# Performance work log

Hardware: AMD Instinct MI355X
Metric: run time of the kernel (lower is better)

The kernel has to match this reference:

```python
import jax, jax.numpy as jnp
import numpy as np

B, N, E, HID, ED, NH = 2, 10000, 160000, 128, 32, 8
HD = HID // NH  # head_dim = 16
EPS = 1e-5


def setup_inputs() -> dict:
    key = jax.random.key(0)
    ks = jax.random.split(key, 12)
    s = 0.05  # keep pre-tanh activations in a sane range
    return {
        "h": jax.random.normal(ks[0], (B, N, HID), jnp.float32),
        "edge_attr": jax.random.normal(ks[1], (B, E, ED), jnp.float32),
        "edge_index": jax.random.randint(ks[2], (E, 2), 0, N),
        "Wq": jax.random.normal(ks[3], (HID, HID), jnp.float32) * s,
        "bq": jnp.zeros((HID,), jnp.float32),
        "Wk": jax.random.normal(ks[4], (HID, HID), jnp.float32) * s,
        "bk": jnp.zeros((HID,), jnp.float32),
        "Wv": jax.random.normal(ks[5], (HID, HID), jnp.float32) * s,
        "bv": jnp.zeros((HID,), jnp.float32),
        "We": jax.random.normal(ks[6], (HID, ED), jnp.float32) * s,
        "be": jnp.zeros((HID,), jnp.float32),
        "attn_vec": jax.random.normal(ks[7], (NH, HD), jnp.float32) * 0.02,
        "Ws": jax.random.normal(ks[8], (HID, HID), jnp.float32) * s,
        "bs": jnp.zeros((HID,), jnp.float32),
        "Wa": jax.random.normal(ks[9], (HID, HID), jnp.float32) * s,
        "ba": jnp.zeros((HID,), jnp.float32),
        "ln_g": jnp.ones((HID,), jnp.float32),
        "ln_b": jnp.zeros((HID,), jnp.float32),
    }


def reference(h, edge_attr, edge_index, Wq, bq, Wk, bk, Wv, bv, We, be,
              attn_vec, Ws, bs, Wa, ba, ln_g, ln_b):
    src = edge_index[:, 0]
    dst = edge_index[:, 1]
    b, n, hid = h.shape
    e_cnt = src.shape[0]

    h_src = h[:, src, :]  # [B,E,HID]
    h_dst = h[:, dst, :]

    q = (h_dst @ Wq.T + bq).reshape(b, e_cnt, NH, HD)
    k = (h_src @ Wk.T + bk).reshape(b, e_cnt, NH, HD)
    v = (h_src @ Wv.T + bv).reshape(b, e_cnt, NH, HD)
    e = (edge_attr @ We.T + be).reshape(b, e_cnt, NH, HD)

    # GATv2-style scores: [B,E,NH]
    logits = jnp.einsum('behd,hd->beh', jnp.tanh(q + k + e), attn_vec)
    logits = logits / np.float32(np.sqrt(HD))

    # segment softmax over edges grouped by dst node (stable)
    lt = jnp.transpose(logits, (1, 0, 2))  # [E,B,NH]
    mx = jax.ops.segment_max(lt, dst, num_segments=n)  # [N,B,NH]
    ex = jnp.exp(lt - mx[dst])
    den = jax.ops.segment_sum(ex, dst, num_segments=n)
    alpha = jnp.transpose(ex / den[dst], (1, 0, 2))  # [B,E,NH]

    msg = (alpha[..., None] * (v + e)).reshape(b, e_cnt, hid)  # [B,E,HID]
    agg = jax.ops.segment_sum(jnp.transpose(msg, (1, 0, 2)), dst, num_segments=n)
    agg = jnp.transpose(agg, (1, 0, 2))  # [B,N,HID]

    update = (h @ Ws.T + bs) + (agg @ Wa.T + ba)
    x = h + jax.nn.gelu(update, approximate=False)  # dropout is identity in eval

    mu = jnp.mean(x, axis=-1, keepdims=True)
    var = jnp.var(x, axis=-1, keepdims=True)
    return (x - mu) / jnp.sqrt(var + EPS) * ln_g + ln_b
```

## Files before the change

kernel.cpp:

```cpp
#include <hip/hip_runtime.h>
#include <math.h>
#include <stdint.h>

#define B_   2
#define N_   10000
#define E_   160000
#define HID_ 128
#define ED_  32
#define NH_  8
#define HD_  16
#define ROWS_ (B_ * N_)

using half2_t = __attribute__((ext_vector_type(2))) _Float16;
using f16x8   = __attribute__((ext_vector_type(8))) _Float16;
using f32x4   = __attribute__((ext_vector_type(4))) float;

__device__ __forceinline__ half2_t f2h2(float a, float b) {
    return __builtin_bit_cast(half2_t, __builtin_amdgcn_cvt_pkrtz(a, b));
}
__device__ __forceinline__ uint32_t pkh2(float a, float b) {
    return __builtin_bit_cast(uint32_t, __builtin_amdgcn_cvt_pkrtz(a, b));
}


__global__ void zero_kernel(int* __restrict__ deg, int* __restrict__ cursor, int n) {
    int i = blockIdx.x * 256 + threadIdx.x;
    if (i < n) { deg[i] = 0; cursor[i] = 0; }
}

__global__ void hist_kernel(const int* __restrict__ ei, int* __restrict__ deg, int E) {
    int e = blockIdx.x * 256 + threadIdx.x;
    if (e < E) atomicAdd(&deg[ei[2 * e + 1]], 1);
}

__global__ __launch_bounds__(256) void scan_kernel(const int* __restrict__ deg,
                                                   int* __restrict__ off, int N) {
    __shared__ int sums[256];
    int t = threadIdx.x;
    int chunk = (N + 255) / 256;
    int s0 = t * chunk, s1 = min(N, s0 + chunk);
    int s = 0;
    for (int i = s0; i < s1; ++i) s += deg[i];
    sums[t] = s;
    __syncthreads();
    #pragma unroll
    for (int d = 1; d < 256; d <<= 1) {
        int v = (t >= d) ? sums[t - d] : 0;
        __syncthreads();
        sums[t] += v;
        __syncthreads();
    }
    if (t == 255) off[N] = sums[255];
    int run = sums[t] - s;
    for (int i = s0; i < s1; ++i) { off[i] = run; run += deg[i]; }
}

__global__ void fill_kernel(const int* __restrict__ ei, const int* __restrict__ off,
                            int* __restrict__ cursor, int* __restrict__ csr, int E) {
    int e = blockIdx.x * 256 + threadIdx.x;
    if (e < E) {
        int d = ei[2 * e + 1];
        int p = atomicAdd(&cursor[d], 1);
        csr[off[d] + p] = e;
    }
}


#define GM 64
#define LDA 68

__global__ __launch_bounds__(256) void qkvs_kernel(
    const float* __restrict__ h,
    const float* __restrict__ Wq, const float* __restrict__ bq,
    const float* __restrict__ Wk, const float* __restrict__ bk,
    const float* __restrict__ Wv, const float* __restrict__ bv,
    const float* __restrict__ Ws, const float* __restrict__ bs,
    const float* __restrict__ ba,
    float* __restrict__ Q, float* __restrict__ KV, float* __restrict__ S)
{
    __shared__ uint32_t As[GM * LDA];
    __shared__ uint32_t Bs[128 * LDA];
    __shared__ float bsm[128];

    int tid = threadIdx.x;
    int lane = tid & 63;
    int wave = tid >> 6;
    int row0 = blockIdx.x * GM;
    int J0 = blockIdx.y * 128;

    if (tid < 128) {
        int J = J0 + tid;
        float v;
        if (J < 128)      v = bq[J];
        else if (J < 256) v = bk[J - 128];
        else if (J < 384) v = bv[J - 256];
        else              v = bs[J - 384] + ba[J - 384];
        bsm[tid] = v;
    }

    for (int f = tid; f < GM * 32; f += 256) {
        int r = f >> 5, c4 = f & 31;
        long row = row0 + r;
        float4 hv = (row < ROWS_) ? *(const float4*)(h + row * HID_ + c4 * 4)
                                  : make_float4(0.f, 0.f, 0.f, 0.f);
        As[r * LDA + c4 * 2]     = pkh2(hv.x, hv.y);
        As[r * LDA + c4 * 2 + 1] = pkh2(hv.z, hv.w);
    }
    for (int f = tid; f < 128 * 32; f += 256) {
        int jr = f >> 5, c4 = f & 31;
        int J = J0 + jr;
        const float* Wp;
        if (J < 128)      Wp = Wq + (long)J * HID_;
        else if (J < 256) Wp = Wk + (long)(J - 128) * HID_;
        else if (J < 384) Wp = Wv + (long)(J - 256) * HID_;
        else              Wp = Ws + (long)(J - 384) * HID_;
        float4 wv = *(const float4*)(Wp + c4 * 4);
        Bs[jr * LDA + c4 * 2]     = pkh2(wv.x, wv.y);
        Bs[jr * LDA + c4 * 2 + 1] = pkh2(wv.z, wv.w);
    }
    __syncthreads();

    f32x4 acc[8];
    #pragma unroll
    for (int nt = 0; nt < 8; ++nt) {
        float c = bsm[nt * 16 + (lane & 15)];
        acc[nt] = (f32x4){ c, c, c, c };
    }

    int ar = wave * 16 + (lane & 15);
    #pragma unroll
    for (int ks = 0; ks < 4; ++ks) {
        f16x8 a = *(const f16x8*)(As + ar * LDA + ks * 16 + (lane >> 4) * 4);
        #pragma unroll
        for (int nt = 0; nt < 8; ++nt) {
            f16x8 b = *(const f16x8*)(Bs + (nt * 16 + (lane & 15)) * LDA + ks * 16 + (lane >> 4) * 4);
            acc[nt] = __builtin_amdgcn_mfma_f32_16x16x32_f16(a, b, acc[nt], 0, 0, 0);
        }
    }

    #pragma unroll
    for (int nt = 0; nt < 8; ++nt) {
        int J = J0 + nt * 16 + (lane & 15);
        long rbase = row0 + wave * 16 + (lane >> 4) * 4;
        #pragma unroll
        for (int r = 0; r < 4; ++r) {
            long row = rbase + r;
            if (row < ROWS_) {
                float v = acc[nt][r];
                if (J < 128)      Q[row * 128 + J] = v;
                else if (J < 256) KV[row * 256 + 2 * (J - 128)] = v;
                else if (J < 384) KV[row * 256 + 2 * (J - 256) + 1] = v;
                else              S[row * 128 + (J - 384)] = v;
            }
        }
    }
}

__global__ __launch_bounds__(256) void wa_kernel(
    const float* __restrict__ X, const float* __restrict__ Wa, float* __restrict__ A)
{
    __shared__ uint32_t As[GM * LDA];
    __shared__ uint32_t Bs[128 * LDA];

    int tid = threadIdx.x;
    int lane = tid & 63;
    int wave = tid >> 6;
    int row0 = blockIdx.x * GM;

    for (int f = tid; f < GM * 32; f += 256) {
        int r = f >> 5, c4 = f & 31;
        long row = row0 + r;
        float4 hv = (row < ROWS_) ? *(const float4*)(X + row * HID_ + c4 * 4)
                                  : make_float4(0.f, 0.f, 0.f, 0.f);
        As[r * LDA + c4 * 2]     = pkh2(hv.x, hv.y);
        As[r * LDA + c4 * 2 + 1] = pkh2(hv.z, hv.w);
    }
    for (int f = tid; f < 128 * 32; f += 256) {
        int jr = f >> 5, c4 = f & 31;
        float4 wv = *(const float4*)(Wa + (long)jr * HID_ + c4 * 4);
        Bs[jr * LDA + c4 * 2]     = pkh2(wv.x, wv.y);
        Bs[jr * LDA + c4 * 2 + 1] = pkh2(wv.z, wv.w);
    }
    __syncthreads();

    f32x4 acc[8];
    #pragma unroll
    for (int nt = 0; nt < 8; ++nt) acc[nt] = (f32x4){ 0.f, 0.f, 0.f, 0.f };

    int ar = wave * 16 + (lane & 15);
    #pragma unroll
    for (int ks = 0; ks < 4; ++ks) {
        f16x8 a = *(const f16x8*)(As + ar * LDA + ks * 16 + (lane >> 4) * 4);
        #pragma unroll
        for (int nt = 0; nt < 8; ++nt) {
            f16x8 b = *(const f16x8*)(Bs + (nt * 16 + (lane & 15)) * LDA + ks * 16 + (lane >> 4) * 4);
            acc[nt] = __builtin_amdgcn_mfma_f32_16x16x32_f16(a, b, acc[nt], 0, 0, 0);
        }
    }

    #pragma unroll
    for (int nt = 0; nt < 8; ++nt) {
        int J = nt * 16 + (lane & 15);
        long rbase = row0 + wave * 16 + (lane >> 4) * 4;
        #pragma unroll
        for (int r = 0; r < 4; ++r) {
            long row = rbase + r;
            if (row < ROWS_) A[row * 128 + J] = acc[nt][r];
        }
    }
}


template <int CTRL>
__device__ __forceinline__ float dpp_add(float x) {
    int y = __builtin_amdgcn_mov_dpp(__float_as_int(x), CTRL, 0xF, 0xF, true);
    return x + __int_as_float(y);
}
__device__ __forceinline__ float hsum16(float p) {
    p = dpp_add<0xB1>(p);
    p = dpp_add<0x4E>(p);
    p = dpp_add<0x141>(p);
    p = dpp_add<0x140>(p);
    return p;
}


#define NPB 2
#define CHUNK 64
#define EAS 20

__global__ __launch_bounds__(128) void node_kernel(
    const float* __restrict__ edge_attr, const int* __restrict__ ei,
    const float* __restrict__ Q, const float* __restrict__ KV,
    const float* __restrict__ We, const float* __restrict__ be,
    const float* __restrict__ attn_vec,
    const int* __restrict__ off, const int* __restrict__ csr,
    float* __restrict__ agg)
{
    int n0 = blockIdx.x * NPB;
    int b  = blockIdx.y;
    int j  = threadIdx.x;
    long bN = (long)b * N_;

    __shared__ int sL[CHUNK];
    __shared__ uint32_t eaL[CHUNK * EAS];

    half2_t we16[16];
    {
        const float4* We4 = (const float4*)(We + (long)j * ED_);
        #pragma unroll
        for (int c = 0; c < 8; ++c) {
            float4 w = We4[c];
            we16[2 * c]     = f2h2(w.x, w.y);
            we16[2 * c + 1] = f2h2(w.z, w.w);
        }
    }
    float bej = be[j];
    float avj = attn_vec[j] * 0.25f;

    float q0 = Q[(bN + n0 + 0) * 128 + j];
    float q1 = Q[(bN + n0 + 1) * 128 + j];

    int o0 = off[n0];
    int c1 = off[n0 + 1] - o0, c2 = off[n0 + 2] - o0;
    int total = c2;

    const float* eab = edge_attr + (long)b * E_ * ED_;
    const float* KVb = KV + bN * 256;

    float acc0 = 0.f, den0 = 0.f, acc1 = 0.f, den1 = 0.f;

    auto edge_body = [&](int i, float qg, float& accg, float& deng) {
        int s = sL[i];
        float2 kv = *(const float2*)(KVb + (long)s * 256 + 2 * j);
        const half2_t* ea = (const half2_t*)(eaL + i * EAS);
        float eja = bej, ejb = 0.f;
        #pragma unroll
        for (int c = 0; c < 8; ++c) {
            eja = __builtin_amdgcn_fdot2(we16[c], ea[c], eja, false);
            ejb = __builtin_amdgcn_fdot2(we16[c + 8], ea[c + 8], ejb, false);
        }
        float ej = eja + ejb;
        float y = qg + kv.x + ej;
        float t = 1.f - 2.f * __builtin_amdgcn_rcpf(__expf(2.f * y) + 1.f);
        float p = hsum16(t * avj);
        float ex = __expf(p);
        deng += ex;
        accg += ex * (kv.y + ej);
    };

    auto range_loop = [&](int lo, int hi, float qg, float& accg, float& deng) {
        int i = lo;
        for (; i + 3 < hi; i += 4) {
            edge_body(i, qg, accg, deng);
            edge_body(i + 1, qg, accg, deng);
            edge_body(i + 2, qg, accg, deng);
            edge_body(i + 3, qg, accg, deng);
        }
        for (; i < hi; ++i) edge_body(i, qg, accg, deng);
    };

    for (int tau = 0; tau < total; tau += CHUNK) {
        int rows = min(total - tau, CHUNK);
        __syncthreads();
        for (int t = j; t < rows; t += 128) {
            int e = csr[o0 + tau + t];
            sL[t] = ei[2 * e];
        }
        for (int idx = j; idx < rows * 8; idx += 128) {
            int r = idx >> 3, c = idx & 7;
            int e = csr[o0 + tau + r];
            float4 f = *(const float4*)(eab + (long)e * ED_ + c * 4);
            eaL[r * EAS + 2 * c]     = pkh2(f.x, f.y);
            eaL[r * EAS + 2 * c + 1] = pkh2(f.z, f.w);
        }
        __syncthreads();

        range_loop(max(0 - tau, 0),  min(c1 - tau, rows), q0, acc0, den0);
        range_loop(max(c1 - tau, 0), min(c2 - tau, rows), q1, acc1, den1);
    }

    agg[(bN + n0 + 0) * 128 + j] = (c1 > 0)  ? acc0 * __builtin_amdgcn_rcpf(den0) : 0.f;
    agg[(bN + n0 + 1) * 128 + j] = (c2 > c1) ? acc1 * __builtin_amdgcn_rcpf(den1) : 0.f;
}


__global__ __launch_bounds__(128) void final_kernel(
    const float* __restrict__ h, const float* __restrict__ S, const float* __restrict__ A,
    const float* __restrict__ ln_g, const float* __restrict__ ln_b,
    float* __restrict__ out)
{
    long row = blockIdx.x;
    int j = threadIdx.x;
    __shared__ float red[4];

    float upd = S[row * 128 + j] + A[row * 128 + j];
    float ge = 0.5f * upd * (1.f + erff(upd * 0.70710678118654752f));
    float x = h[row * 128 + j] + ge;

    float s = x, s2 = x * x;
    #pragma unroll
    for (int m = 1; m < 64; m <<= 1) { s += __shfl_xor(s, m); s2 += __shfl_xor(s2, m); }
    int wv = j >> 6;
    if ((j & 63) == 0) { red[wv] = s; red[2 + wv] = s2; }
    __syncthreads();
    float Sm = red[0] + red[1], S2m = red[2] + red[3];
    float mu = Sm * (1.f / 128.f);
    float var = S2m * (1.f / 128.f) - mu * mu;
    out[row * 128 + j] = (x - mu) * rsqrtf(var + 1e-5f) * ln_g[j] + ln_b[j];
}


extern "C" void kernel_launch(void* const* d_in, const int* in_sizes, int n_in,
                              void* d_out, int out_size, void* d_ws, size_t ws_size,
                              hipStream_t stream) {
    const float* h         = (const float*)d_in[0];
    const float* edge_attr = (const float*)d_in[1];
    const int*   ei        = (const int*)  d_in[2];
    const float* Wq = (const float*)d_in[3];
    const float* bq = (const float*)d_in[4];
    const float* Wk = (const float*)d_in[5];
    const float* bk = (const float*)d_in[6];
    const float* Wv = (const float*)d_in[7];
    const float* bv = (const float*)d_in[8];
    const float* We = (const float*)d_in[9];
    const float* be = (const float*)d_in[10];
    const float* attn_vec = (const float*)d_in[11];
    const float* Ws = (const float*)d_in[12];
    const float* bs = (const float*)d_in[13];
    const float* Wa = (const float*)d_in[14];
    const float* ba = (const float*)d_in[15];
    const float* ln_g = (const float*)d_in[16];
    const float* ln_b = (const float*)d_in[17];
    float* out = (float*)d_out;

    size_t p = 0;
    auto alloc = [&](size_t bytes) { size_t r = p; p += (bytes + 255) & ~(size_t)255; return r; };
    char* ws = (char*)d_ws;
    float* Q    = (float*)(ws + alloc((size_t)ROWS_ * 128 * 4));
    float* KV   = (float*)(ws + alloc((size_t)ROWS_ * 256 * 4));
    float* S    = (float*)(ws + alloc((size_t)ROWS_ * 128 * 4));
    float* agg  = (float*)(ws + alloc((size_t)ROWS_ * 128 * 4));
    int* deg    = (int*)(ws + alloc((size_t)N_ * 4));
    int* cursor = (int*)(ws + alloc((size_t)N_ * 4));
    int* off    = (int*)(ws + alloc((size_t)(N_ + 1) * 4));
    int* csr    = (int*)(ws + alloc((size_t)E_ * 4));
    float* A = Q;
    (void)ws_size;

    zero_kernel<<<(N_ + 255) / 256, 256, 0, stream>>>(deg, cursor, N_);
    hist_kernel<<<(E_ + 255) / 256, 256, 0, stream>>>(ei, deg, E_);
    scan_kernel<<<1, 256, 0, stream>>>(deg, off, N_);
    fill_kernel<<<(E_ + 255) / 256, 256, 0, stream>>>(ei, off, cursor, csr, E_);

    dim3 ggrid((ROWS_ + GM - 1) / GM, 4);
    qkvs_kernel<<<ggrid, 256, 0, stream>>>(h, Wq, bq, Wk, bk, Wv, bv, Ws, bs, ba,
                                           Q, KV, S);

    dim3 grid(N_ / NPB, B_);
    node_kernel<<<grid, 128, 0, stream>>>(edge_attr, ei, Q, KV, We, be, attn_vec,
                                          off, csr, agg);

    dim3 wgrid((ROWS_ + GM - 1) / GM, 1);
    wa_kernel<<<wgrid, 256, 0, stream>>>(agg, Wa, A);

    final_kernel<<<ROWS_, 128, 0, stream>>>(h, S, A, ln_g, ln_b, out);
}
```

Measured before the change: 177.5 us.

## Precompute edge projections with MFMA per batch and store K/V in fp16

Adds an MFMA-based eproj kernel that computes edge_attr @ We^T + be once per edge into an fp16 buffer, run per batch and followed by a per-batch node kernel. The node kernel no longer recomputes the 32-wide edge projection per edge per thread with fdot2. It reads a single fp16 value per edge instead. K/V are also stored as packed fp16, halving gather bandwidth, and the shared-memory chunk is enlarged. This trades per-edge ALU work for an extra 40MB-per-batch fp16 write and reread, extra launches, and reduced precision in the gathered values.

```diff
diff --git a/kernel.cpp b/kernel.cpp
--- a/kernel.cpp
+++ b/kernel.cpp
@@ -15,11 +15,11 @@
 using f16x8   = __attribute__((ext_vector_type(8))) _Float16;
 using f32x4   = __attribute__((ext_vector_type(4))) float;
 
-__device__ __forceinline__ half2_t f2h2(float a, float b) {
-    return __builtin_bit_cast(half2_t, __builtin_amdgcn_cvt_pkrtz(a, b));
-}
 __device__ __forceinline__ uint32_t pkh2(float a, float b) {
     return __builtin_bit_cast(uint32_t, __builtin_amdgcn_cvt_pkrtz(a, b));
+}
+__device__ __forceinline__ uint16_t f2h(float v) {
+    return __builtin_bit_cast(uint16_t, (_Float16)v);
 }
 
 
@@ -76,7 +76,7 @@
     const float* __restrict__ Wv, const float* __restrict__ bv,
     const float* __restrict__ Ws, const float* __restrict__ bs,
     const float* __restrict__ ba,
-    float* __restrict__ Q, float* __restrict__ KV, float* __restrict__ S)
+    float* __restrict__ Q, uint16_t* __restrict__ KVh, float* __restrict__ S)
 {
     __shared__ uint32_t As[GM * LDA];
     __shared__ uint32_t Bs[128 * LDA];
@@ -148,13 +148,150 @@
             if (row < ROWS_) {
                 float v = acc[nt][r];
                 if (J < 128)      Q[row * 128 + J] = v;
-                else if (J < 256) KV[row * 256 + 2 * (J - 128)] = v;
-                else if (J < 384) KV[row * 256 + 2 * (J - 256) + 1] = v;
+                else if (J < 256) KVh[row * 256 + 2 * (J - 128)] = f2h(v);
+                else if (J < 384) KVh[row * 256 + 2 * (J - 256) + 1] = f2h(v);
                 else              S[row * 128 + (J - 384)] = v;
             }
         }
     }
 }
+
+
+#define EM 64
+#define ELD 18
+
+__global__ __launch_bounds__(256) void eproj_kernel(
+    const float* __restrict__ ea,
+    const float* __restrict__ We, const float* __restrict__ be,
+    uint16_t* __restrict__ Ep)
+{
+    __shared__ uint32_t As[EM * ELD];
+    __shared__ uint32_t Bs[128 * ELD];
+    __shared__ float bsm[128];
+
+    int tid = threadIdx.x;
+    int lane = tid & 63;
+    int wave = tid >> 6;
+    long row0 = (long)blockIdx.x * EM;
+
+    if (tid < 128) bsm[tid] = be[tid];
+
+    for (int f = tid; f < EM * 8; f += 256) {
+        int r = f >> 3, c4 = f & 7;
+        float4 v = *(const float4*)(ea + (row0 + r) * ED_ + c4 * 4);
+        As[r * ELD + c4 * 2]     = pkh2(v.x, v.y);
+        As[r * ELD + c4 * 2 + 1] = pkh2(v.z, v.w);
+    }
+    for (int f = tid; f < 128 * 8; f += 256) {
+        int r = f >> 3, c4 = f & 7;
+        float4 v = *(const float4*)(We + (long)r * ED_ + c4 * 4);
+        Bs[r * ELD + c4 * 2]     = pkh2(v.x, v.y);
+        Bs[r * ELD + c4 * 2 + 1] = pkh2(v.z, v.w);
+    }
+    __syncthreads();
+
+    int ar = wave * 16 + (lane & 15);
+    f16x8 a = *(const f16x8*)(As + ar * ELD + (lane >> 4) * 4);
+    long rbase = row0 + wave * 16 + (lane >> 4) * 4;
+    #pragma unroll
+    for (int nt = 0; nt < 8; ++nt) {
+        float c = bsm[nt * 16 + (lane & 15)];
+        f32x4 acc = (f32x4){ c, c, c, c };
+        f16x8 b = *(const f16x8*)(Bs + (nt * 16 + (lane & 15)) * ELD + (lane >> 4) * 4);
+        acc = __builtin_amdgcn_mfma_f32_16x16x32_f16(a, b, acc, 0, 0, 0);
+        int pcol = nt * 16 + (lane & 15);
+        #pragma unroll
+        for (int r = 0; r < 4; ++r)
+            Ep[(rbase + r) * 128 + pcol] = f2h(acc[r]);
+    }
+}
+
+
+template <int CTRL>
+__device__ __forceinline__ float dpp_add(float x) {
+    int y = __builtin_amdgcn_mov_dpp(__float_as_int(x), CTRL, 0xF, 0xF, true);
+    return x + __int_as_float(y);
+}
+__device__ __forceinline__ float hsum16(float p) {
+    p = dpp_add<0xB1>(p);
+    p = dpp_add<0x4E>(p);
+    p = dpp_add<0x141>(p);
+    p = dpp_add<0x140>(p);
+    return p;
+}
+
+
+#define NPB 2
+#define CHUNK 128
+
+__global__ __launch_bounds__(128) void node_kernel(
+    const int* __restrict__ ei,
+    const float* __restrict__ Q, const uint32_t* __restrict__ KVp,
+    const uint16_t* __restrict__ Ep,
+    const float* __restrict__ attn_vec,
+    const int* __restrict__ off, const int* __restrict__ csr,
+    float* __restrict__ agg, int b)
+{
+    int n0 = blockIdx.x * NPB;
+    int j  = threadIdx.x;
+    long bN = (long)b * N_;
+
+    __shared__ int sL[CHUNK], eL[CHUNK];
+
+    float avj = attn_vec[j] * 0.25f;
+
+    float q0 = Q[(bN + n0 + 0) * 128 + j];
+    float q1 = Q[(bN + n0 + 1) * 128 + j];
+
+    int o0 = off[n0];
+    int c1 = off[n0 + 1] - o0, c2 = off[n0 + 2] - o0;
+    int total = c2;
+
+    const uint32_t* KVb = KVp + bN * 128;
+
+    float acc0 = 0.f, den0 = 0.f, acc1 = 0.f, den1 = 0.f;
+
+    auto edge_body = [&](int i, float qg, float& accg, float& deng) {
+        int s = sL[i], e = eL[i];
+        half2_t kv = __builtin_bit_cast(half2_t, KVb[(long)s * 128 + j]);
+        float ej = (float)__builtin_bit_cast(_Float16, Ep[(long)e * 128 + j]);
+        float y = qg + (float)kv.x + ej;
+        float t = 1.f - 2.f * __builtin_amdgcn_rcpf(__expf(2.f * y) + 1.f);
+        float p = hsum16(t * avj);
+        float ex = __expf(p);
+        deng += ex;
+        accg += ex * ((float)kv.y + ej);
+    };
+
+    auto range_loop = [&](int lo, int hi, float qg, float& accg, float& deng) {
+        int i = lo;
+        for (; i + 3 < hi; i += 4) {
+            edge_body(i, qg, accg, deng);
+            edge_body(i + 1, qg, accg, deng);
+            edge_body(i + 2, qg, accg, deng);
+            edge_body(i + 3, qg, accg, deng);
+        }
+        for (; i < hi; ++i) edge_body(i, qg, accg, deng);
+    };
+
+    for (int tau = 0; tau < total; tau += CHUNK) {
+        int rows = min(total - tau, CHUNK);
+        __syncthreads();
+        if (j < rows) {
+            int e = csr[o0 + tau + j];
+            eL[j] = e;
+            sL[j] = ei[2 * e];
+        }
+        __syncthreads();
+
+        range_loop(max(0 - tau, 0),  min(c1 - tau, rows), q0, acc0, den0);
+        range_loop(max(c1 - tau, 0), min(c2 - tau, rows), q1, acc1, den1);
+    }
+
+    agg[(bN + n0 + 0) * 128 + j] = (c1 > 0)  ? acc0 * __builtin_amdgcn_rcpf(den0) : 0.f;
+    agg[(bN + n0 + 1) * 128 + j] = (c2 > c1) ? acc1 * __builtin_amdgcn_rcpf(den1) : 0.f;
+}
+
 
 __global__ __launch_bounds__(256) void wa_kernel(
     const float* __restrict__ X, const float* __restrict__ Wa, float* __restrict__ A)
@@ -208,120 +345,6 @@
             if (row < ROWS_) A[row * 128 + J] = acc[nt][r];
         }
     }
-}
-
-
-template <int CTRL>
-__device__ __forceinline__ float dpp_add(float x) {
-    int y = __builtin_amdgcn_mov_dpp(__float_as_int(x), CTRL, 0xF, 0xF, true);
-    return x + __int_as_float(y);
-}
-__device__ __forceinline__ float hsum16(float p) {
-    p = dpp_add<0xB1>(p);
-    p = dpp_add<0x4E>(p);
-    p = dpp_add<0x141>(p);
-    p = dpp_add<0x140>(p);
-    return p;
-}
-
-
-#define NPB 2
-#define CHUNK 64
-#define EAS 20
-
-__global__ __launch_bounds__(128) void node_kernel(
-    const float* __restrict__ edge_attr, const int* __restrict__ ei,
-    const float* __restrict__ Q, const float* __restrict__ KV,
-    const float* __restrict__ We, const float* __restrict__ be,
-    const float* __restrict__ attn_vec,
-    const int* __restrict__ off, const int* __restrict__ csr,
-    float* __restrict__ agg)
-{
-    int n0 = blockIdx.x * NPB;
-    int b  = blockIdx.y;
-    int j  = threadIdx.x;
-    long bN = (long)b * N_;
-
-    __shared__ int sL[CHUNK];
-    __shared__ uint32_t eaL[CHUNK * EAS];
-
-    half2_t we16[16];
-    {
-        const float4* We4 = (const float4*)(We + (long)j * ED_);
-        #pragma unroll
-        for (int c = 0; c < 8; ++c) {
-            float4 w = We4[c];
-            we16[2 * c]     = f2h2(w.x, w.y);
-            we16[2 * c + 1] = f2h2(w.z, w.w);
-        }
-    }
-    float bej = be[j];
-    float avj = attn_vec[j] * 0.25f;
-
-    float q0 = Q[(bN + n0 + 0) * 128 + j];
-    float q1 = Q[(bN + n0 + 1) * 128 + j];
-
-    int o0 = off[n0];
-    int c1 = off[n0 + 1] - o0, c2 = off[n0 + 2] - o0;
-    int total = c2;
-
-    const float* eab = edge_attr + (long)b * E_ * ED_;
-    const float* KVb = KV + bN * 256;
-
-    float acc0 = 0.f, den0 = 0.f, acc1 = 0.f, den1 = 0.f;
-
-    auto edge_body = [&](int i, float qg, float& accg, float& deng) {
-        int s = sL[i];
-        float2 kv = *(const float2*)(KVb + (long)s * 256 + 2 * j);
-        const half2_t* ea = (const half2_t*)(eaL + i * EAS);
-        float eja = bej, ejb = 0.f;
-        #pragma unroll
-        for (int c = 0; c < 8; ++c) {
-            eja = __builtin_amdgcn_fdot2(we16[c], ea[c], eja, false);
-            ejb = __builtin_amdgcn_fdot2(we16[c + 8], ea[c + 8], ejb, false);
-        }
-        float ej = eja + ejb;
-        float y = qg + kv.x + ej;
-        float t = 1.f - 2.f * __builtin_amdgcn_rcpf(__expf(2.f * y) + 1.f);
-        float p = hsum16(t * avj);
-        float ex = __expf(p);
-        deng += ex;
-        accg += ex * (kv.y + ej);
-    };
-
-    auto range_loop = [&](int lo, int hi, float qg, float& accg, float& deng) {
-        int i = lo;
-        for (; i + 3 < hi; i += 4) {
-            edge_body(i, qg, accg, deng);
-            edge_body(i + 1, qg, accg, deng);
-            edge_body(i + 2, qg, accg, deng);
-            edge_body(i + 3, qg, accg, deng);
-        }
-        for (; i < hi; ++i) edge_body(i, qg, accg, deng);
-    };
-
-    for (int tau = 0; tau < total; tau += CHUNK) {
-        int rows = min(total - tau, CHUNK);
-        __syncthreads();
-        for (int t = j; t < rows; t += 128) {
-            int e = csr[o0 + tau + t];
-            sL[t] = ei[2 * e];
-        }
-        for (int idx = j; idx < rows * 8; idx += 128) {
-            int r = idx >> 3, c = idx & 7;
-            int e = csr[o0 + tau + r];
-            float4 f = *(const float4*)(eab + (long)e * ED_ + c * 4);
-            eaL[r * EAS + 2 * c]     = pkh2(f.x, f.y);
-            eaL[r * EAS + 2 * c + 1] = pkh2(f.z, f.w);
-        }
-        __syncthreads();
-
-        range_loop(max(0 - tau, 0),  min(c1 - tau, rows), q0, acc0, den0);
-        range_loop(max(c1 - tau, 0), min(c2 - tau, rows), q1, acc1, den1);
-    }
-
-    agg[(bN + n0 + 0) * 128 + j] = (c1 > 0)  ? acc0 * __builtin_amdgcn_rcpf(den0) : 0.f;
-    agg[(bN + n0 + 1) * 128 + j] = (c2 > c1) ? acc1 * __builtin_amdgcn_rcpf(den1) : 0.f;
 }
 
 
@@ -377,10 +400,11 @@
     size_t p = 0;
     auto alloc = [&](size_t bytes) { size_t r = p; p += (bytes + 255) & ~(size_t)255; return r; };
     char* ws = (char*)d_ws;
-    float* Q    = (float*)(ws + alloc((size_t)ROWS_ * 128 * 4));
-    float* KV   = (float*)(ws + alloc((size_t)ROWS_ * 256 * 4));
-    float* S    = (float*)(ws + alloc((size_t)ROWS_ * 128 * 4));
-    float* agg  = (float*)(ws + alloc((size_t)ROWS_ * 128 * 4));
+    float*    Q    = (float*)(ws + alloc((size_t)ROWS_ * 128 * 4));
+    uint16_t* KVh  = (uint16_t*)(ws + alloc((size_t)ROWS_ * 256 * 2));
+    float*    S    = (float*)(ws + alloc((size_t)ROWS_ * 128 * 4));
+    float*    agg  = (float*)(ws + alloc((size_t)ROWS_ * 128 * 4));
+    uint16_t* Ep   = (uint16_t*)(ws + alloc((size_t)E_ * 128 * 2));
     int* deg    = (int*)(ws + alloc((size_t)N_ * 4));
     int* cursor = (int*)(ws + alloc((size_t)N_ * 4));
     int* off    = (int*)(ws + alloc((size_t)(N_ + 1) * 4));
@@ -395,14 +419,16 @@
 
     dim3 ggrid((ROWS_ + GM - 1) / GM, 4);
     qkvs_kernel<<<ggrid, 256, 0, stream>>>(h, Wq, bq, Wk, bk, Wv, bv, Ws, bs, ba,
-                                           Q, KV, S);
-
-    dim3 grid(N_ / NPB, B_);
-    node_kernel<<<grid, 128, 0, stream>>>(edge_attr, ei, Q, KV, We, be, attn_vec,
-                                          off, csr, agg);
-
-    dim3 wgrid((ROWS_ + GM - 1) / GM, 1);
-    wa_kernel<<<wgrid, 256, 0, stream>>>(agg, Wa, A);
+                                           Q, KVh, S);
+
+    for (int b = 0; b < B_; ++b) {
+        eproj_kernel<<<E_ / EM, 256, 0, stream>>>(edge_attr + (size_t)b * E_ * ED_,
+                                                  We, be, Ep);
+        node_kernel<<<N_ / NPB, 128, 0, stream>>>(ei, Q, (const uint32_t*)KVh, Ep,
+                                                  attn_vec, off, csr, agg, b);
+    }
+
+    wa_kernel<<<(ROWS_ + GM - 1) / GM, 256, 0, stream>>>(agg, Wa, A);
 
     final_kernel<<<ROWS_, 128, 0, stream>>>(h, S, A, ln_g, ln_b, out);
 }
```

Result: slower. 181.6 us (+2.4%).
